# Kernel tuning notes

Hardware: AMD Instinct MI355X
Metric: run time of the kernel (lower is better)

## Reference

```python
import jax, jax.numpy as jnp
import numpy as np

N_NODES = 200_000
N_EVENTS = 50_000
MEM = 128
RAW = 64
TD = 64
HEADS = 2
DH = MEM // HEADS
EDGE_DIM = RAW + TD
MSG_IN = 2 * MEM + RAW + TD


def _time_enc(x, w, b):
    # PyG TimeEncoder: cos(Linear(t)) with Linear(1, time_dim)
    return jnp.cos(x[..., None] * w + b)


def setup_inputs() -> dict:
    key = jax.random.key(0)
    ks = jax.random.split(key, 30)

    def w(i, shape, scale=None):
        s = scale if scale is not None else 1.0 / np.sqrt(shape[-1])
        return jax.random.normal(ks[i], shape, jnp.float32) * s

    src = jax.random.randint(ks[0], (N_EVENTS,), 0, N_NODES)
    dst = jax.random.randint(ks[1], (N_EVENTS,), 0, N_NODES)
    t = jnp.sort(jax.random.uniform(ks[2], (N_EVENTS,), jnp.float32, 0.0, 1e4))
    return dict(
        memory=w(3, (N_NODES, MEM), 1.0),
        last_update=jnp.zeros((N_NODES,), jnp.float32),
        t=t,
        msg=w(4, (N_EVENTS, RAW), 1.0),
        src=src, dst=dst,
        time_w=w(5, (TD,), 1.0), time_b=w(6, (TD,), 1.0),
        gru_Wih=w(7, (3 * MEM, MSG_IN)), gru_bih=w(8, (3 * MEM,), 0.02),
        gru_Whh=w(9, (3 * MEM, MEM)), gru_bhh=w(10, (3 * MEM,), 0.02),
        Wq=w(11, (MEM, MEM)), bq=w(12, (MEM,), 0.02),
        Wk=w(13, (MEM, MEM)), bk=w(14, (MEM,), 0.02),
        Wv=w(15, (MEM, MEM)), bv=w(16, (MEM,), 0.02),
        We=w(17, (MEM, EDGE_DIM)),
        Wskip=w(18, (MEM, MEM)), bskip=w(19, (MEM,), 0.02),
        Wls=w(20, (MEM, MEM)), bls=w(21, (MEM,), 0.02),
        Wld=w(22, (MEM, MEM)), bld=w(23, (MEM,), 0.02),
        Wlf=w(24, (1, MEM)), blf=w(25, (1,), 0.02),
    )


def reference(memory, last_update, t, msg, src, dst, time_w, time_b,
              gru_Wih, gru_bih, gru_Whh, gru_bhh,
              Wq, bq, Wk, bk, Wv, bv, We, Wskip, bskip,
              Wls, bls, Wld, bld, Wlf, blf):
    N, D = memory.shape
    E = src.shape[0]
    # --- 1. IdentityMessage: raw store for src side and dst side of each event ---
    dt_s = t - last_update[src]
    dt_d = t - last_update[dst]
    m_s = jnp.concatenate([memory[src], memory[dst], msg, _time_enc(dt_s, time_w, time_b)], -1)
    m_d = jnp.concatenate([memory[dst], memory[src], msg, _time_enc(dt_d, time_w, time_b)], -1)
    all_msg = jnp.concatenate([m_s, m_d], 0)        # [2E, MSG_IN]
    all_id = jnp.concatenate([src, dst], 0)         # [2E]
    all_t = jnp.concatenate([t, t], 0)              # [2E]
    # --- 2. LastAggregator: keep the latest message per target node ---
    pos = jnp.arange(2 * E, dtype=jnp.int32)
    last_pos = jnp.full((N,), -1, jnp.int32).at[all_id].max(pos)
    is_last = last_pos[all_id] == pos               # [2E], exactly one True per touched node
    # --- 3. GRUCell memory update (computed per message, scattered for the last one) ---
    h = memory[all_id]
    gi = all_msg @ gru_Wih.T + gru_bih
    gh = h @ gru_Whh.T + gru_bhh
    ir, iz, i_n = jnp.split(gi, 3, -1)
    hr, hz, h_n = jnp.split(gh, 3, -1)
    r = jax.nn.sigmoid(ir + hr)
    zg = jax.nn.sigmoid(iz + hz)
    n = jnp.tanh(i_n + r * h_n)
    h_new = (1.0 - zg) * n + zg * h
    memory_new = memory.at[all_id].add(jnp.where(is_last[:, None], h_new - h, 0.0))
    last_update_new = last_update.at[all_id].max(jnp.where(is_last, all_t, -jnp.inf))
    # --- 4. GraphAttentionEmbedding: TransformerConv(heads=2, edge_dim) in eval mode ---
    rel_t = last_update_new[src] - t
    edge_attr = jnp.concatenate([_time_enc(rel_t, time_w, time_b), msg], -1)  # [E, EDGE_DIM]
    e_proj = edge_attr @ We.T                                                  # [E, MEM]
    q = (memory_new @ Wq.T + bq).reshape(N, HEADS, DH)
    k = (memory_new[src] @ Wk.T + bk + e_proj).reshape(E, HEADS, DH)
    v = (memory_new[src] @ Wv.T + bv + e_proj).reshape(E, HEADS, DH)
    logit = jnp.einsum('ehd,ehd->eh', q[dst], k) / np.sqrt(DH).astype(np.float32)
    mx = jnp.full((N, HEADS), -jnp.inf, memory.dtype).at[dst].max(logit)
    a = jnp.exp(logit - mx[dst])
    denom = jax.ops.segment_sum(a, dst, num_segments=N)
    attn = a / denom[dst]                                                      # segment softmax over incoming edges
    out = jnp.zeros((N, HEADS, DH), memory.dtype).at[dst].add(attn[..., None] * v)
    z = out.reshape(N, D) + memory_new @ Wskip.T + bskip                       # root/skip connection
    # --- 5. LinkPredictor on event endpoints ---
    hlp = jax.nn.relu(z[src] @ Wls.T + bls + z[dst] @ Wld.T + bld)
    return hlp @ Wlf.T + blf                                                   # [E, 1]
```

## Files before the change

kernel.cpp:

```cpp
#include <hip/hip_runtime.h>
#include <math.h>

#define NN 200000
#define NE 50000
#define D 128
#define ZROW 256

#define WGRU_SZ  196608
#define WATTN_SZ 147456
#define WLNK2_SZ 65536

__device__ __forceinline__ float frcp_(float x) { return __builtin_amdgcn_rcpf(x); }
__device__ __forceinline__ float fsig_(float x) { return frcp_(1.f + __expf(-x)); }
__device__ __forceinline__ float ftanh_(float x) {
    float xc = fminf(fmaxf(x, -15.f), 15.f);
    float t = __expf(2.f * xc);
    return (t - 1.f) * frcp_(t + 1.f);
}

__device__ __forceinline__ unsigned short f2bf(float f) {
    unsigned int u = __float_as_uint(f);
    u = (u + 0x7fffu + ((u >> 16) & 1u)) >> 16;
    return (unsigned short)u;
}
__device__ __forceinline__ float bf2f(unsigned short b) {
    return __uint_as_float(((unsigned int)b) << 16);
}

typedef short bf16x8 __attribute__((ext_vector_type(8)));
typedef float f32x4  __attribute__((ext_vector_type(4)));

__global__ void k_initprep(const float* __restrict__ Wih, const float* __restrict__ Whh,
                           const float* __restrict__ Wk, const float* __restrict__ Wv,
                           const float* __restrict__ Wq, const float* __restrict__ We,
                           const float* __restrict__ Wskip, const float* __restrict__ bskip,
                           const float* __restrict__ Wls, const float* __restrict__ Wld,
                           const float* __restrict__ bls, const float* __restrict__ bld,
                           const int* __restrict__ src, const int* __restrict__ dst,
                           unsigned short* __restrict__ wgru,
                           unsigned short* __restrict__ wattn,
                           unsigned short* __restrict__ wlink2,
                           float* __restrict__ blink,
                           int* __restrict__ last_pos, int* __restrict__ count) {
    int idx = blockIdx.x * 256 + threadIdx.x;
    if (idx == 0) *count = 0;
    if (idx < 2 * NE) {
        int id = (idx < NE) ? src[idx] : dst[idx - NE];
        atomicMax(&last_pos[id], idx + 1);
    }
    if (idx >= 102528) return;
    float4 v;
    unsigned short* dstp;
    int ncopies, stride;
    if (idx < 49152) {
        int n = idx / 96;
        int c = (idx - n * 96) * 4;
        if (n < 384) {
            v = *(const float4*)&Wih[n * 384 + c];
            if (n < 256 && c < 128) {
                const float4 w2 = *(const float4*)&Whh[n * 128 + c];
                v.x += w2.x; v.y += w2.y; v.z += w2.z; v.w += w2.w;
            }
        } else {
            if (c >= 128) return;
            v = *(const float4*)&Whh[(n - 128) * 128 + c];
        }
        dstp = &wgru[n * 384 + c]; ncopies = 8; stride = WGRU_SZ;
    } else if (idx < 49152 + 36864) {
        int i2 = idx - 49152;
        int n = i2 / 96;
        int c = (i2 - n * 96) * 4;
        if (n < 256) {
            const float* Wm = (n < 128) ? Wk : Wv;
            int nn = n & 127;
            if (c < 128)       v = *(const float4*)&Wm[nn * 128 + c];
            else if (c < 256)  v = *(const float4*)&We[nn * 128 + (c - 128)];
            else return;
        } else {
            if (c < 256) return;
            v = *(const float4*)&Wq[(n - 256) * 128 + (c - 256)];
        }
        dstp = &wattn[n * 384 + c]; ncopies = 4; stride = WATTN_SZ;
    } else if (idx < 86016 + 8192) {
        int i4 = idx - 86016;
        int n = i4 >> 6;
        int c = (i4 & 63) * 4;
        int dc;
        if (c < 128) { v = *(const float4*)&Wls[n * 128 + c];        dc = c; }
        else         { v = *(const float4*)&Wld[n * 128 + (c - 128)]; dc = c + 128; }
        dstp = &wlink2[n * 512 + dc]; ncopies = 4; stride = WLNK2_SZ;
    } else if (idx < 94208 + 8192) {
        int i5 = idx - 94208;
        int n = i5 >> 6;
        int g = i5 & 63;
        const float* Wrow = (g < 32) ? &Wls[n * 128] : &Wld[n * 128];
        int c = (g & 31) * 4;
        float ax = 0.f, ay = 0.f, az = 0.f, aw = 0.f;
        for (int j = 0; j < 128; ++j) {
            float a = Wrow[j];
            const float4 ws = *(const float4*)&Wskip[j * 128 + c];
            ax += a * ws.x; ay += a * ws.y; az += a * ws.z; aw += a * ws.w;
        }
        ushort4 b4;
        b4.x = f2bf(ax); b4.y = f2bf(ay); b4.z = f2bf(az); b4.w = f2bf(aw);
        unsigned short* dp = &wlink2[n * 512 + ((g < 32) ? 128 : 384) + c];
        for (int r = 0; r < 4; ++r)
            *(ushort4*)(dp + (size_t)r * WLNK2_SZ) = b4;
        return;
    } else {
        int n = idx - 102400;
        float s = bls[n] + bld[n];
        for (int j = 0; j < 128; ++j)
            s += (Wls[n * 128 + j] + Wld[n * 128 + j]) * bskip[j];
        blink[n] = s;
        return;
    }
    ushort4 b;
    b.x = f2bf(v.x); b.y = f2bf(v.y); b.z = f2bf(v.z); b.w = f2bf(v.w);
    for (int r = 0; r < ncopies; ++r)
        *(ushort4*)(dstp + (size_t)r * stride) = b;
}

__global__ void k_compact(const int* __restrict__ src, const int* __restrict__ dst,
                          const int* __restrict__ last_pos,
                          int* __restrict__ count, int* __restrict__ clist,
                          int* __restrict__ node2slot, int* __restrict__ head) {
    int i = blockIdx.x * blockDim.x + threadIdx.x;
    if (i < 2 * NE) {
        int id = (i < NE) ? src[i] : dst[i - NE];
        if (last_pos[id] == i + 1) {
            int s = atomicAdd(count, 1);
            clist[s] = i;
            node2slot[id] = s;
            head[s] = -1;
        }
    }
}

#define GMB 64
__global__ __launch_bounds__(512, 4) void k_gru(
    const float* __restrict__ memp, const float* __restrict__ lup,
    const float* __restrict__ tp, const float* __restrict__ msgp,
    const int* __restrict__ srcp, const int* __restrict__ dstp,
    const float* __restrict__ twp, const float* __restrict__ tbp,
    const int* __restrict__ clist,
    const unsigned short* __restrict__ wgru_all,
    const float* __restrict__ bih, const float* __restrict__ bhh,
    const int* __restrict__ countp,
    unsigned short* __restrict__ zcat,
    float* __restrict__ lu_new)
{
    __shared__ alignas(16) unsigned short Xs[64][392];
    __shared__ int sid[64], sother[64], se[64];
    __shared__ float sdt[64];
    int cnt = *countp;
    int base = blockIdx.x * GMB;
    if (base >= cnt) return;
    int tid = threadIdx.x;
    const unsigned short* __restrict__ wgru = wgru_all + (size_t)(blockIdx.x & 7) * WGRU_SZ;

    if (tid < 64) {
        int ii = base + tid;
        bool valid = ii < cnt;
        int iw = clist[valid ? ii : (cnt - 1)];
        int e = (iw < NE) ? iw : (iw - NE);
        int id    = (iw < NE) ? srcp[e] : dstp[e];
        int oth   = (iw < NE) ? dstp[e] : srcp[e];
        sid[tid] = id; sother[tid] = oth; se[tid] = e;
        float tt = tp[e];
        float lu = lup[id];
        sdt[tid] = tt - lu;
        if (valid) lu_new[id] = fmaxf(lu, tt);
    }
    __syncthreads();
    {
        int m = tid >> 3, li = tid & 7;
        int id = sid[m], oth = sother[m], e = se[m];
        float dt = sdt[m];
        #pragma unroll
        for (int j = 0; j < 12; ++j) {
            int c4 = li + 8 * j;
            float4 v;
            if (c4 < 32)      v = *(const float4*)&memp[id * D + c4 * 4];
            else if (c4 < 64) v = *(const float4*)&memp[oth * D + (c4 - 32) * 4];
            else if (c4 < 80) v = *(const float4*)&msgp[e * 64 + (c4 - 64) * 4];
            else {
                int c0 = (c4 - 80) * 4;
                v.x = cosf(dt * twp[c0 + 0] + tbp[c0 + 0]);
                v.y = cosf(dt * twp[c0 + 1] + tbp[c0 + 1]);
                v.z = cosf(dt * twp[c0 + 2] + tbp[c0 + 2]);
                v.w = cosf(dt * twp[c0 + 3] + tbp[c0 + 3]);
            }
            ushort4 b;
            b.x = f2bf(v.x); b.y = f2bf(v.y); b.z = f2bf(v.z); b.w = f2bf(v.w);
            *(ushort4*)&Xs[m][c4 * 4] = b;
        }
    }
    __syncthreads();

    int lane = tid & 63, w = tid >> 6;
    int q = lane >> 4, l15 = lane & 15;
    int q8 = q * 8, w16 = w * 16;

    f32x4 acc[4][4];
    #pragma unroll
    for (int mt = 0; mt < 4; ++mt)
        #pragma unroll
        for (int g = 0; g < 4; ++g)
            acc[mt][g] = (f32x4)(0.0f);

#define GRU_STEP(NG)                                                                      \
    {                                                                                     \
        bf16x8 a[4];                                                                      \
        _Pragma("unroll")                                                                 \
        for (int mt = 0; mt < 4; ++mt) a[mt] = *(const bf16x8*)&Xs[mt * 16 + l15][k0 + q8]; \
        _Pragma("unroll")                                                                 \
        for (int g = 0; g < NG; ++g) {                                                    \
            const bf16x8 b = *(const bf16x8*)&wgru[(g * 128 + w16 + l15) * 384 + k0 + q8]; \
            _Pragma("unroll")                                                             \
            for (int mt = 0; mt < 4; ++mt)                                                \
                acc[mt][g] = __builtin_amdgcn_mfma_f32_16x16x32_bf16(a[mt], b, acc[mt][g], 0, 0, 0); \
        }                                                                                 \
    }

    #pragma unroll 2
    for (int ks = 0; ks < 4; ++ks) { int k0 = ks * 32; GRU_STEP(4) }
    #pragma unroll 2
    for (int ks = 4; ks < 12; ++ks) { int k0 = ks * 32; GRU_STEP(3) }
#undef GRU_STEP

    float nval[4][4];
    {
        int c = w16 + l15;
        float br  = bih[c]       + bhh[c];
        float bz  = bih[128 + c] + bhh[128 + c];
        float bin = bih[256 + c];
        float bhn = bhh[256 + c];
        #pragma unroll
        for (int mt = 0; mt < 4; ++mt) {
            #pragma unroll
            for (int reg = 0; reg < 4; ++reg) {
                int m = mt * 16 + q * 4 + reg;
                float r  = fsig_(acc[mt][0][reg] + br);
                float zg = fsig_(acc[mt][1][reg] + bz);
                float n  = ftanh_(acc[mt][2][reg] + bin + r * (acc[mt][3][reg] + bhn));
                float hv = bf2f(Xs[m][c]);
                nval[mt][reg] = (1.f - zg) * n + zg * hv;
            }
        }
    }

    __syncthreads();
    {
        int c = w16 + l15;
        #pragma unroll
        for (int mt = 0; mt < 4; ++mt)
            #pragma unroll
            for (int reg = 0; reg < 4; ++reg)
                Xs[mt * 16 + q * 4 + reg][c] = f2bf(nval[mt][reg]);
    }
    __syncthreads();

    {
        #pragma unroll
        for (int j = 0; j < 2; ++j) {
            int ch = tid + 512 * j;
            int m = ch >> 4, c8 = ch & 15;
            *(uint4*)&zcat[(size_t)(base + m) * ZROW + 128 + c8 * 8] =
                *(const uint4*)&Xs[m][c8 * 8];
        }
    }
}

#define AMB 32
__global__ __launch_bounds__(256) void k_attnA(
    const int* __restrict__ srcp, const int* __restrict__ dstp,
    const float* __restrict__ tp, const float* __restrict__ msgp,
    const float* __restrict__ twp, const float* __restrict__ tbp,
    const float* __restrict__ lu_new, const int* __restrict__ node2slot,
    const unsigned short* __restrict__ zcat,
    const unsigned short* __restrict__ wattn_all,
    const float* __restrict__ bq, const float* __restrict__ bk, const float* __restrict__ bv,
    unsigned short* __restrict__ vbuf, float* __restrict__ abuf,
    int* __restrict__ head, int* __restrict__ next)
{
    __shared__ alignas(16) unsigned short Xs[32][392];
    unsigned short (*kLb)[136] = (unsigned short(*)[136])(&Xs[0][0]);
    unsigned short (*qLb)[136] = (unsigned short(*)[136])(&Xs[0][0] + 4352);
    __shared__ float sa[AMB][2];
    __shared__ int sslot[AMB], sdslot[AMB];
    __shared__ float srel[AMB];
    int tid = threadIdx.x;
    int e0 = blockIdx.x * AMB;
    const unsigned short* __restrict__ wattn = wattn_all + (size_t)(blockIdx.x & 3) * WATTN_SZ;
    {
        int gid = blockIdx.x * 256 + tid;
        if (gid < NE) {
            int sl = node2slot[dstp[gid]];
            next[gid] = atomicExch(&head[sl], gid);
        }
    }
    if (tid < AMB) {
        int e = e0 + tid; if (e >= NE) e = NE - 1;
        int s = srcp[e], dd = dstp[e];
        sslot[tid]  = node2slot[s];
        sdslot[tid] = node2slot[dd];
        srel[tid] = lu_new[s] - tp[e];
    }
    __syncthreads();
    {
        int m = tid >> 3, li = tid & 7;
        int e = e0 + m; if (e >= NE) e = NE - 1;
        int ssl = sslot[m], dsl = sdslot[m];
        float rel = srel[m];
        uint4* xrow = (uint4*)&Xs[m][0];
        const uint4* srow = (const uint4*)&zcat[(size_t)ssl * ZROW + 128];
        const uint4* drow = (const uint4*)&zcat[(size_t)dsl * ZROW + 128];
        #pragma unroll
        for (int j = 0; j < 2; ++j) {
            xrow[li + 8 * j]      = srow[li + 8 * j];
            xrow[32 + li + 8 * j] = drow[li + 8 * j];
        }
        {
            int c0 = li * 8;
            ushort4 lo, hi;
            lo.x = f2bf(cosf(rel * twp[c0 + 0] + tbp[c0 + 0]));
            lo.y = f2bf(cosf(rel * twp[c0 + 1] + tbp[c0 + 1]));
            lo.z = f2bf(cosf(rel * twp[c0 + 2] + tbp[c0 + 2]));
            lo.w = f2bf(cosf(rel * twp[c0 + 3] + tbp[c0 + 3]));
            hi.x = f2bf(cosf(rel * twp[c0 + 4] + tbp[c0 + 4]));
            hi.y = f2bf(cosf(rel * twp[c0 + 5] + tbp[c0 + 5]));
            hi.z = f2bf(cosf(rel * twp[c0 + 6] + tbp[c0 + 6]));
            hi.w = f2bf(cosf(rel * twp[c0 + 7] + tbp[c0 + 7]));
            *(ushort4*)&Xs[m][128 + c0]     = lo;
            *(ushort4*)&Xs[m][128 + c0 + 4] = hi;
        }
        {
            float4 a = *(const float4*)&msgp[e * 64 + li * 8];
            float4 b = *(const float4*)&msgp[e * 64 + li * 8 + 4];
            ushort4 lo, hi;
            lo.x = f2bf(a.x); lo.y = f2bf(a.y); lo.z = f2bf(a.z); lo.w = f2bf(a.w);
            hi.x = f2bf(b.x); hi.y = f2bf(b.y); hi.z = f2bf(b.z); hi.w = f2bf(b.w);
            *(ushort4*)&Xs[m][192 + li * 8]     = lo;
            *(ushort4*)&Xs[m][192 + li * 8 + 4] = hi;
        }
    }
    __syncthreads();

    int lane = tid & 63, w = tid >> 6;
    int q = lane >> 4, l15 = lane & 15;
    int q8 = q * 8;

    f32x4 acc[2][6];
    #pragma unroll
    for (int mt = 0; mt < 2; ++mt)
        #pragma unroll
        for (int jj = 0; jj < 6; ++jj) acc[mt][jj] = (f32x4)(0.0f);

    #pragma unroll 2
    for (int ks = 0; ks < 8; ++ks) {
        int k0 = ks * 32;
        const bf16x8 a0 = *(const bf16x8*)&Xs[l15][k0 + q8];
        const bf16x8 a1 = *(const bf16x8*)&Xs[16 + l15][k0 + q8];
        #pragma unroll
        for (int jj = 0; jj < 4; ++jj) {
            int nt = w + 4 * jj;
            const bf16x8 b = *(const bf16x8*)&wattn[(nt * 16 + l15) * 384 + k0 + q8];
            acc[0][jj] = __builtin_amdgcn_mfma_f32_16x16x32_bf16(a0, b, acc[0][jj], 0, 0, 0);
            acc[1][jj] = __builtin_amdgcn_mfma_f32_16x16x32_bf16(a1, b, acc[1][jj], 0, 0, 0);
        }
    }
    #pragma unroll 2
    for (int ks = 8; ks < 12; ++ks) {
        int k0 = ks * 32;
        const bf16x8 a0 = *(const bf16x8*)&Xs[l15][k0 + q8];
        const bf16x8 a1 = *(const bf16x8*)&Xs[16 + l15][k0 + q8];
        #pragma unroll
        for (int jj = 4; jj < 6; ++jj) {
            int nt = w + 4 * jj;
            const bf16x8 b = *(const bf16x8*)&wattn[(nt * 16 + l15) * 384 + k0 + q8];
            acc[0][jj] = __builtin_amdgcn_mfma_f32_16x16x32_bf16(a0, b, acc[0][jj], 0, 0, 0);
            acc[1][jj] = __builtin_amdgcn_mfma_f32_16x16x32_bf16(a1, b, acc[1][jj], 0, 0, 0);
        }
    }

    __syncthreads();

    float vreg[2][2][4];
    #pragma unroll
    for (int jj = 0; jj < 6; ++jj) {
        int nt = w + 4 * jj;
        int gate = nt >> 3;
        int ch = (nt & 7) * 16 + l15;
        float bias = (gate == 0) ? bk[ch] : (gate == 1) ? bv[ch] : bq[ch];
        #pragma unroll
        for (int mt = 0; mt < 2; ++mt)
            #pragma unroll
            for (int reg = 0; reg < 4; ++reg) {
                int m = mt * 16 + q * 4 + reg;
                float val = acc[mt][jj][reg] + bias;
                if (gate == 0)      kLb[m][ch] = f2bf(val);
                else if (gate == 2) qLb[m][ch] = f2bf(val);
                else                vreg[jj - 2][mt][reg] = val;
            }
    }
    __syncthreads();
    #pragma unroll
    for (int pr = 0; pr < 16; ++pr) {
        int p2 = pr * 4 + w;
        int m = p2 >> 1, h = p2 & 1;
        float prod = bf2f(qLb[m][h * 64 + lane]) * bf2f(kLb[m][h * 64 + lane]);
        #pragma unroll
        for (int off = 32; off; off >>= 1) prod += __shfl_down(prod, off);
        if (lane == 0) {
            float a = __expf(prod * 0.125f);
            sa[m][h] = a;
            if (e0 + m < NE) abuf[(e0 + m) * 2 + h] = a;
        }
    }
    __syncthreads();
    {
        unsigned short (*vL)[136] = qLb;
        #pragma unroll
        for (int jv = 0; jv < 2; ++jv) {
            int ch = w * 16 + jv * 64 + l15;
            int h = jv;
            #pragma unroll
            for (int mt = 0; mt < 2; ++mt)
                #pragma unroll
                for (int reg = 0; reg < 4; ++reg) {
                    int m = mt * 16 + q * 4 + reg;
                    vL[m][ch] = f2bf(sa[m][h] * vreg[jv][mt][reg]);
                }
        }
        __syncthreads();
        #pragma unroll
        for (int j = 0; j < 2; ++j) {
            int chunk = tid + 256 * j;
            int row = chunk >> 4, c8 = chunk & 15;
            if (e0 + row < NE)
                *(uint4*)&vbuf[(size_t)(e0 + row) * D + c8 * 8] = *(const uint4*)&vL[row][c8 * 8];
        }
    }
}

__global__ __launch_bounds__(256) void k_gather(
    const int* __restrict__ countp, const int* __restrict__ head,
    const int* __restrict__ next, const float* __restrict__ abuf,
    const unsigned short* __restrict__ vbuf, unsigned short* __restrict__ zcat)
{
    int cnt = *countp;
    int slot = blockIdx.x * 32 + (threadIdx.x >> 3);
    if (slot >= cnt) return;
    int li = threadIdx.x & 7;
    int c0 = li * 16;
    int h = li >> 2;
    float vsum[16];
    #pragma unroll
    for (int j = 0; j < 16; ++j) vsum[j] = 0.f;
    float asum = 0.f;
    for (int e = head[slot]; e != -1; e = next[e]) {
        asum += abuf[e * 2 + h];
        uint4 v0 = *(const uint4*)&vbuf[(size_t)e * D + c0];
        uint4 v1 = *(const uint4*)&vbuf[(size_t)e * D + c0 + 8];
        const unsigned short* pv0 = (const unsigned short*)&v0;
        const unsigned short* pv1 = (const unsigned short*)&v1;
        #pragma unroll
        for (int j = 0; j < 8; ++j) { vsum[j] += bf2f(pv0[j]); vsum[8 + j] += bf2f(pv1[j]); }
    }
    float rr = (asum > 0.f) ? frcp_(asum) : 0.f;
    unsigned short o[16];
    #pragma unroll
    for (int j = 0; j < 16; ++j) o[j] = f2bf(vsum[j] * rr);
    *(uint4*)&zcat[(size_t)slot * ZROW + c0]     = *(const uint4*)&o[0];
    *(uint4*)&zcat[(size_t)slot * ZROW + c0 + 8] = *(const uint4*)&o[8];
}

#define ALB 64
__global__ __launch_bounds__(256) void k_link(
    const int* __restrict__ srcp, const int* __restrict__ dstp,
    const int* __restrict__ node2slot,
    const unsigned short* __restrict__ zcat,
    const unsigned short* __restrict__ wlink2_all,
    const float* __restrict__ blink,
    const float* __restrict__ Wlf, const float* __restrict__ blf,
    float* __restrict__ outp)
{
    __shared__ alignas(16) unsigned short Xs[64][520];
    __shared__ int ssl[64], sdl[64];
    __shared__ float sred[64][4];
    int tid = threadIdx.x;
    int e0 = blockIdx.x * ALB;
    const unsigned short* __restrict__ wlink2 = wlink2_all + (size_t)(blockIdx.x & 3) * WLNK2_SZ;
    if (tid < ALB) {
        int e = e0 + tid; if (e >= NE) e = NE - 1;
        ssl[tid] = node2slot[srcp[e]];
        sdl[tid] = node2slot[dstp[e]];
    }
    __syncthreads();
    {
        int m = tid >> 2, li = tid & 3;
        uint4* xrow = (uint4*)&Xs[m][0];
        const uint4* srow = (const uint4*)&zcat[(size_t)ssl[m] * ZROW];
        const uint4* drow = (const uint4*)&zcat[(size_t)sdl[m] * ZROW];
        #pragma unroll
        for (int j = 0; j < 8; ++j) {
            xrow[li + 4 * j]      = srow[li + 4 * j];
            xrow[32 + li + 4 * j] = drow[li + 4 * j];
        }
    }
    __syncthreads();

    int lane = tid & 63, w = tid >> 6;
    int q = lane >> 4, l15 = lane & 15;
    int q8 = q * 8;

    f32x4 acc[4][2];
    #pragma unroll
    for (int mt = 0; mt < 4; ++mt)
        #pragma unroll
        for (int jj = 0; jj < 2; ++jj) acc[mt][jj] = (f32x4)(0.0f);

    #pragma unroll 2
    for (int ks = 0; ks < 16; ++ks) {
        int k0 = ks * 32;
        bf16x8 a[4];
        #pragma unroll
        for (int mt = 0; mt < 4; ++mt) a[mt] = *(const bf16x8*)&Xs[mt * 16 + l15][k0 + q8];
        #pragma unroll
        for (int jj = 0; jj < 2; ++jj) {
            int nt = w + 4 * jj;
            const bf16x8 b = *(const bf16x8*)&wlink2[(nt * 16 + l15) * 512 + k0 + q8];
            #pragma unroll
            for (int mt = 0; mt < 4; ++mt)
                acc[mt][jj] = __builtin_amdgcn_mfma_f32_16x16x32_bf16(a[mt], b, acc[mt][jj], 0, 0, 0);
        }
    }

    float p[4][4];
    #pragma unroll
    for (int mt = 0; mt < 4; ++mt)
        #pragma unroll
        for (int reg = 0; reg < 4; ++reg) p[mt][reg] = 0.f;
    #pragma unroll
    for (int jj = 0; jj < 2; ++jj) {
        int ch = (w + 4 * jj) * 16 + l15;
        float bias = blink[ch];
        float wl = Wlf[ch];
        #pragma unroll
        for (int mt = 0; mt < 4; ++mt)
            #pragma unroll
            for (int reg = 0; reg < 4; ++reg)
                p[mt][reg] += fmaxf(acc[mt][jj][reg] + bias, 0.f) * wl;
    }
    #pragma unroll
    for (int mask = 1; mask < 16; mask <<= 1) {
        #pragma unroll
        for (int mt = 0; mt < 4; ++mt)
            #pragma unroll
            for (int reg = 0; reg < 4; ++reg)
                p[mt][reg] += __shfl_xor(p[mt][reg], mask);
    }
    if (l15 == 0) {
        #pragma unroll
        for (int mt = 0; mt < 4; ++mt)
            #pragma unroll
            for (int reg = 0; reg < 4; ++reg)
                sred[mt * 16 + q * 4 + reg][w] = p[mt][reg];
    }
    __syncthreads();
    if (tid < ALB) {
        int e = e0 + tid;
        if (e < NE)
            outp[e] = sred[tid][0] + sred[tid][1] + sred[tid][2] + sred[tid][3] + blf[0];
    }
}

extern "C" void kernel_launch(void* const* d_in, const int* in_sizes, int n_in,
                              void* d_out, int out_size, void* d_ws, size_t ws_size,
                              hipStream_t stream)
{
    const float* memory      = (const float*)d_in[0];
    const float* last_update = (const float*)d_in[1];
    const float* t           = (const float*)d_in[2];
    const float* msg         = (const float*)d_in[3];
    const int*   src         = (const int*)d_in[4];
    const int*   dst         = (const int*)d_in[5];
    const float* time_w      = (const float*)d_in[6];
    const float* time_b      = (const float*)d_in[7];
    const float* gru_Wih     = (const float*)d_in[8];
    const float* gru_bih     = (const float*)d_in[9];
    const float* gru_Whh     = (const float*)d_in[10];
    const float* gru_bhh     = (const float*)d_in[11];
    const float* Wq          = (const float*)d_in[12];
    const float* bq          = (const float*)d_in[13];
    const float* Wk          = (const float*)d_in[14];
    const float* bk          = (const float*)d_in[15];
    const float* Wv          = (const float*)d_in[16];
    const float* bv          = (const float*)d_in[17];
    const float* We          = (const float*)d_in[18];
    const float* Wskip       = (const float*)d_in[19];
    const float* bskip       = (const float*)d_in[20];
    const float* Wls         = (const float*)d_in[21];
    const float* bls         = (const float*)d_in[22];
    const float* Wld         = (const float*)d_in[23];
    const float* bld         = (const float*)d_in[24];
    const float* Wlf         = (const float*)d_in[25];
    const float* blf         = (const float*)d_in[26];
    float* outp = (float*)d_out;

    char* ws = (char*)d_ws;
    int*   last_pos  = (int*)  (ws + 0);
    int*   node2slot = (int*)  (ws + 800000);
    float* lu_new    = (float*)(ws + 1600000);
    int*   count     = (int*)  (ws + 2400000);
    int*   clist     = (int*)  (ws + 2400016);
    unsigned short* wlink2  = (unsigned short*)(ws + 2800016);
    float* blink   = (float*)(ws + 3324304);
    unsigned short* wgru    = (unsigned short*)(ws + 79624592);
    unsigned short* wattn   = (unsigned short*)(ws + 82770320);
    unsigned short* zcat    = (unsigned short*)(ws + 84474256);
    unsigned short* vbuf    = (unsigned short*)(ws + 135690640);
    float* abuf = (float*)(ws + 148490640);
    int*   head = (int*)  (ws + 148890640);
    int*   next = (int*)  (ws + 149290768);

    k_initprep<<<401, 256, 0, stream>>>(
                 gru_Wih, gru_Whh, Wk, Wv, Wq, We, Wskip, bskip, Wls, Wld, bls, bld,
                 src, dst, wgru, wattn, wlink2, blink, last_pos, count);
    k_compact <<<(2 * NE + 255) / 256, 256, 0, stream>>>(src, dst, last_pos, count,
                 clist, node2slot, head);
    k_gru     <<<(2 * NE + GMB - 1) / GMB, 512, 0, stream>>>(memory, last_update, t, msg,
                 src, dst, time_w, time_b, clist, wgru, gru_bih, gru_bhh,
                 count, zcat, lu_new);
    k_attnA   <<<(NE + AMB - 1) / AMB, 256, 0, stream>>>(src, dst, t, msg, time_w, time_b,
                 lu_new, node2slot, zcat, wattn, bq, bk, bv, vbuf, abuf, head, next);
    k_gather  <<<(2 * NE + 31) / 32, 256, 0, stream>>>(count, head, next, abuf, vbuf, zcat);
    k_link    <<<(NE + ALB - 1) / ALB, 256, 0, stream>>>(src, dst, node2slot, zcat,
                 wlink2, blink, Wlf, blf, outp);
}
```

Measured before the change: 400.9 us.

## Precompute bf16 memory rows per slot in compact; halve link tile size

The compact kernel now writes each unique node's memory row as bf16 into a slot-indexed buffer, plus per-slot aux data (event, other node, dt, id), and updates lu_new itself. The GRU kernel then gathers bf16 rows by slot for both the node and its partner through node2slot, instead of reading fp32 memory and converting it. This removes the clist indirection and one sync. The link kernel's event tile shrinks from 64 to 32 rows to launch more blocks. The trade-off is one serial thread per slot copying a 512-byte row in compact, and a dependence on every partner node having a slot, which holds because both endpoints of every event are compacted.

```diff
diff --git a/kernel.cpp b/kernel.cpp
--- a/kernel.cpp
+++ b/kernel.cpp
@@ -123,78 +123,88 @@
 
 __global__ void k_compact(const int* __restrict__ src, const int* __restrict__ dst,
                           const int* __restrict__ last_pos,
-                          int* __restrict__ count, int* __restrict__ clist,
-                          int* __restrict__ node2slot, int* __restrict__ head) {
+                          const float* __restrict__ memory,
+                          const float* __restrict__ tp, const float* __restrict__ lup,
+                          int* __restrict__ count, int* __restrict__ node2slot,
+                          int* __restrict__ head,
+                          unsigned short* __restrict__ mco,
+                          int4* __restrict__ slot_aux,
+                          float* __restrict__ lu_new) {
     int i = blockIdx.x * blockDim.x + threadIdx.x;
-    if (i < 2 * NE) {
-        int id = (i < NE) ? src[i] : dst[i - NE];
-        if (last_pos[id] == i + 1) {
-            int s = atomicAdd(count, 1);
-            clist[s] = i;
-            node2slot[id] = s;
-            head[s] = -1;
-        }
+    if (i >= 2 * NE) return;
+    int e  = (i < NE) ? i : i - NE;
+    int id = (i < NE) ? src[e] : dst[e];
+    if (last_pos[id] != i + 1) return;
+    int s = atomicAdd(count, 1);
+    node2slot[id] = s;
+    head[s] = -1;
+    int oth = (i < NE) ? dst[e] : src[e];
+    float tt = tp[e];
+    float lu = lup[id];
+    lu_new[id] = fmaxf(lu, tt);
+    int4 aux; aux.x = e; aux.y = oth; aux.z = __float_as_int(tt - lu); aux.w = id;
+    slot_aux[s] = aux;
+    const float4* mrow = (const float4*)(memory + (size_t)id * D);
+    ushort4* orow = (ushort4*)(mco + (size_t)s * D);
+    #pragma unroll 8
+    for (int j = 0; j < 32; ++j) {
+        float4 v = mrow[j];
+        ushort4 b;
+        b.x = f2bf(v.x); b.y = f2bf(v.y); b.z = f2bf(v.z); b.w = f2bf(v.w);
+        orow[j] = b;
     }
 }
 
 #define GMB 64
-__global__ __launch_bounds__(512, 4) void k_gru(
-    const float* __restrict__ memp, const float* __restrict__ lup,
-    const float* __restrict__ tp, const float* __restrict__ msgp,
-    const int* __restrict__ srcp, const int* __restrict__ dstp,
+__global__ __launch_bounds__(512) void k_gru(
+    const float* __restrict__ msgp,
     const float* __restrict__ twp, const float* __restrict__ tbp,
-    const int* __restrict__ clist,
+    const int4* __restrict__ slot_aux, const int* __restrict__ node2slot,
+    const unsigned short* __restrict__ mco,
     const unsigned short* __restrict__ wgru_all,
     const float* __restrict__ bih, const float* __restrict__ bhh,
     const int* __restrict__ countp,
-    unsigned short* __restrict__ zcat,
-    float* __restrict__ lu_new)
+    unsigned short* __restrict__ zcat)
 {
     __shared__ alignas(16) unsigned short Xs[64][392];
-    __shared__ int sid[64], sother[64], se[64];
-    __shared__ float sdt[64];
     int cnt = *countp;
     int base = blockIdx.x * GMB;
     if (base >= cnt) return;
     int tid = threadIdx.x;
     const unsigned short* __restrict__ wgru = wgru_all + (size_t)(blockIdx.x & 7) * WGRU_SZ;
 
-    if (tid < 64) {
-        int ii = base + tid;
-        bool valid = ii < cnt;
-        int iw = clist[valid ? ii : (cnt - 1)];
-        int e = (iw < NE) ? iw : (iw - NE);
-        int id    = (iw < NE) ? srcp[e] : dstp[e];
-        int oth   = (iw < NE) ? dstp[e] : srcp[e];
-        sid[tid] = id; sother[tid] = oth; se[tid] = e;
-        float tt = tp[e];
-        float lu = lup[id];
-        sdt[tid] = tt - lu;
-        if (valid) lu_new[id] = fmaxf(lu, tt);
-    }
-    __syncthreads();
     {
         int m = tid >> 3, li = tid & 7;
-        int id = sid[m], oth = sother[m], e = se[m];
-        float dt = sdt[m];
-        #pragma unroll
-        for (int j = 0; j < 12; ++j) {
-            int c4 = li + 8 * j;
-            float4 v;
-            if (c4 < 32)      v = *(const float4*)&memp[id * D + c4 * 4];
-            else if (c4 < 64) v = *(const float4*)&memp[oth * D + (c4 - 32) * 4];
-            else if (c4 < 80) v = *(const float4*)&msgp[e * 64 + (c4 - 64) * 4];
-            else {
-                int c0 = (c4 - 80) * 4;
-                v.x = cosf(dt * twp[c0 + 0] + tbp[c0 + 0]);
-                v.y = cosf(dt * twp[c0 + 1] + tbp[c0 + 1]);
-                v.z = cosf(dt * twp[c0 + 2] + tbp[c0 + 2]);
-                v.w = cosf(dt * twp[c0 + 3] + tbp[c0 + 3]);
-            }
-            ushort4 b;
-            b.x = f2bf(v.x); b.y = f2bf(v.y); b.z = f2bf(v.z); b.w = f2bf(v.w);
-            *(ushort4*)&Xs[m][c4 * 4] = b;
-        }
+        int ii = base + m; if (ii >= cnt) ii = cnt - 1;
+        const int4 aux = slot_aux[ii];
+        int e = aux.x, oth = aux.y;
+        float dt = __int_as_float(aux.z);
+        int osl = node2slot[oth];
+        const uint4* idr  = (const uint4*)(mco + (size_t)ii  * D);
+        const uint4* othr = (const uint4*)(mco + (size_t)osl * D);
+        uint4 A0 = idr[li],  A1 = idr[li + 8];
+        uint4 B0 = othr[li], B1 = othr[li + 8];
+        float4 M0 = *(const float4*)&msgp[e * 64 + li * 8];
+        float4 M1 = *(const float4*)&msgp[e * 64 + li * 8 + 4];
+        int c0 = li * 8;
+        float cv[8];
+        #pragma unroll
+        for (int k = 0; k < 8; ++k)
+            cv[k] = cosf(dt * twp[c0 + k] + tbp[c0 + k]);
+        *(uint4*)&Xs[m][li * 8]        = A0;
+        *(uint4*)&Xs[m][64 + li * 8]   = A1;
+        *(uint4*)&Xs[m][128 + li * 8]  = B0;
+        *(uint4*)&Xs[m][192 + li * 8]  = B1;
+        ushort4 lo, hi;
+        lo.x = f2bf(M0.x); lo.y = f2bf(M0.y); lo.z = f2bf(M0.z); lo.w = f2bf(M0.w);
+        hi.x = f2bf(M1.x); hi.y = f2bf(M1.y); hi.z = f2bf(M1.z); hi.w = f2bf(M1.w);
+        *(ushort4*)&Xs[m][256 + c0]     = lo;
+        *(ushort4*)&Xs[m][256 + c0 + 4] = hi;
+        ushort4 t0, t1;
+        t0.x = f2bf(cv[0]); t0.y = f2bf(cv[1]); t0.z = f2bf(cv[2]); t0.w = f2bf(cv[3]);
+        t1.x = f2bf(cv[4]); t1.y = f2bf(cv[5]); t1.z = f2bf(cv[6]); t1.w = f2bf(cv[7]);
+        *(ushort4*)&Xs[m][320 + c0]     = t0;
+        *(ushort4*)&Xs[m][320 + c0 + 4] = t1;
     }
     __syncthreads();
 
@@ -476,7 +486,7 @@
     *(uint4*)&zcat[(size_t)slot * ZROW + c0 + 8] = *(const uint4*)&o[8];
 }
 
-#define ALB 64
+#define ALB 32
 __global__ __launch_bounds__(256) void k_link(
     const int* __restrict__ srcp, const int* __restrict__ dstp,
     const int* __restrict__ node2slot,
@@ -486,9 +496,9 @@
     const float* __restrict__ Wlf, const float* __restrict__ blf,
     float* __restrict__ outp)
 {
-    __shared__ alignas(16) unsigned short Xs[64][520];
-    __shared__ int ssl[64], sdl[64];
-    __shared__ float sred[64][4];
+    __shared__ alignas(16) unsigned short Xs[32][520];
+    __shared__ int ssl[32], sdl[32];
+    __shared__ float sred[32][4];
     int tid = threadIdx.x;
     int e0 = blockIdx.x * ALB;
     const unsigned short* __restrict__ wlink2 = wlink2_all + (size_t)(blockIdx.x & 3) * WLNK2_SZ;
@@ -499,14 +509,14 @@
     }
     __syncthreads();
     {
-        int m = tid >> 2, li = tid & 3;
+        int m = tid >> 3, li = tid & 7;
         uint4* xrow = (uint4*)&Xs[m][0];
         const uint4* srow = (const uint4*)&zcat[(size_t)ssl[m] * ZROW];
         const uint4* drow = (const uint4*)&zcat[(size_t)sdl[m] * ZROW];
         #pragma unroll
-        for (int j = 0; j < 8; ++j) {
-            xrow[li + 4 * j]      = srow[li + 4 * j];
-            xrow[32 + li + 4 * j] = drow[li + 4 * j];
+        for (int j = 0; j < 4; ++j) {
+            xrow[li + 8 * j]      = srow[li + 8 * j];
+            xrow[32 + li + 8 * j] = drow[li + 8 * j];
         }
     }
     __syncthreads();
@@ -515,31 +525,31 @@
     int q = lane >> 4, l15 = lane & 15;
     int q8 = q * 8;
 
-    f32x4 acc[4][2];
-    #pragma unroll
-    for (int mt = 0; mt < 4; ++mt)
+    f32x4 acc[2][2];
+    #pragma unroll
+    for (int mt = 0; mt < 2; ++mt)
         #pragma unroll
         for (int jj = 0; jj < 2; ++jj) acc[mt][jj] = (f32x4)(0.0f);
 
     #pragma unroll 2
     for (int ks = 0; ks < 16; ++ks) {
         int k0 = ks * 32;
-        bf16x8 a[4];
-        #pragma unroll
-        for (int mt = 0; mt < 4; ++mt) a[mt] = *(const bf16x8*)&Xs[mt * 16 + l15][k0 + q8];
+        bf16x8 a[2];
+        #pragma unroll
+        for (int mt = 0; mt < 2; ++mt) a[mt] = *(const bf16x8*)&Xs[mt * 16 + l15][k0 + q8];
         #pragma unroll
         for (int jj = 0; jj < 2; ++jj) {
             int nt = w + 4 * jj;
             const bf16x8 b = *(const bf16x8*)&wlink2[(nt * 16 + l15) * 512 + k0 + q8];
             #pragma unroll
-            for (int mt = 0; mt < 4; ++mt)
+            for (int mt = 0; mt < 2; ++mt)
                 acc[mt][jj] = __builtin_amdgcn_mfma_f32_16x16x32_bf16(a[mt], b, acc[mt][jj], 0, 0, 0);
         }
     }
 
-    float p[4][4];
-    #pragma unroll
-    for (int mt = 0; mt < 4; ++mt)
+    float p[2][4];
+    #pragma unroll
+    for (int mt = 0; mt < 2; ++mt)
         #pragma unroll
         for (int reg = 0; reg < 4; ++reg) p[mt][reg] = 0.f;
     #pragma unroll
@@ -548,7 +558,7 @@
         float bias = blink[ch];
         float wl = Wlf[ch];
         #pragma unroll
-        for (int mt = 0; mt < 4; ++mt)
+        for (int mt = 0; mt < 2; ++mt)
             #pragma unroll
             for (int reg = 0; reg < 4; ++reg)
                 p[mt][reg] += fmaxf(acc[mt][jj][reg] + bias, 0.f) * wl;
@@ -556,14 +566,14 @@
     #pragma unroll
     for (int mask = 1; mask < 16; mask <<= 1) {
         #pragma unroll
-        for (int mt = 0; mt < 4; ++mt)
+        for (int mt = 0; mt < 2; ++mt)
             #pragma unroll
             for (int reg = 0; reg < 4; ++reg)
                 p[mt][reg] += __shfl_xor(p[mt][reg], mask);
     }
     if (l15 == 0) {
         #pragma unroll
-        for (int mt = 0; mt < 4; ++mt)
+        for (int mt = 0; mt < 2; ++mt)
             #pragma unroll
             for (int reg = 0; reg < 4; ++reg)
                 sred[mt * 16 + q * 4 + reg][w] = p[mt][reg];
@@ -614,9 +624,10 @@
     int*   node2slot = (int*)  (ws + 800000);
     float* lu_new    = (float*)(ws + 1600000);
     int*   count     = (int*)  (ws + 2400000);
-    int*   clist     = (int*)  (ws + 2400016);
     unsigned short* wlink2  = (unsigned short*)(ws + 2800016);
     float* blink   = (float*)(ws + 3324304);
+    unsigned short* mco     = (unsigned short*)(ws + 4000000);
+    int4*  slot_aux = (int4*)(ws + 30000000);
     unsigned short* wgru    = (unsigned short*)(ws + 79624592);
     unsigned short* wattn   = (unsigned short*)(ws + 82770320);
     unsigned short* zcat    = (unsigned short*)(ws + 84474256);
@@ -628,11 +639,10 @@
     k_initprep<<<401, 256, 0, stream>>>(
                  gru_Wih, gru_Whh, Wk, Wv, Wq, We, Wskip, bskip, Wls, Wld, bls, bld,
                  src, dst, wgru, wattn, wlink2, blink, last_pos, count);
-    k_compact <<<(2 * NE + 255) / 256, 256, 0, stream>>>(src, dst, last_pos, count,
-                 clist, node2slot, head);
-    k_gru     <<<(2 * NE + GMB - 1) / GMB, 512, 0, stream>>>(memory, last_update, t, msg,
-                 src, dst, time_w, time_b, clist, wgru, gru_bih, gru_bhh,
-                 count, zcat, lu_new);
+    k_compact <<<(2 * NE + 255) / 256, 256, 0, stream>>>(src, dst, last_pos, memory,
+                 t, last_update, count, node2slot, head, mco, slot_aux, lu_new);
+    k_gru     <<<(2 * NE + GMB - 1) / GMB, 512, 0, stream>>>(msg, time_w, time_b,
+                 slot_aux, node2slot, mco, wgru, gru_bih, gru_bhh, count, zcat);
     k_attnA   <<<(NE + AMB - 1) / AMB, 256, 0, stream>>>(src, dst, t, msg, time_w, time_b,
                  lu_new, node2slot, zcat, wattn, bq, bk, bv, vbuf, abuf, head, next);
     k_gather  <<<(2 * NE + 31) / 32, 256, 0, stream>>>(count, head, next, abuf, vbuf, zcat);
```

New measurement: 432.5 us. 1.08x slower.
